# Performance work log

Hardware: AMD Instinct MI355X
Metric: run time of the kernel (lower is better)

The kernel has to match this reference:

```python
import jax, jax.numpy as jnp
import numpy as np
import math

HID = 2048; NH = 16; NKV = 4; NG = NH // NKV
LORA = 512; D_ROPE = 64; D_NOPE = 128; D_V = 128
D_QK = D_NOPE + D_ROPE  # 192
B, S = 2, 2048
ROPE_BASE = 10000.0


def setup_inputs() -> dict:
    key = jax.random.key(0)
    ks = jax.random.split(key, 5)
    s = lambda fan_in: 1.0 / math.sqrt(fan_in)
    return {
        "hidden_states": jax.random.normal(ks[0], (B, S, HID), jnp.float32),
        "Wqkv": jax.random.uniform(ks[1], (HID, NH * D_QK + LORA), jnp.float32, -s(HID), s(HID)),
        "Wk_up": jax.random.uniform(ks[2], (LORA, NKV * D_QK), jnp.float32, -s(LORA), s(LORA)),
        "Wv_up": jax.random.uniform(ks[3], (LORA, NKV * D_V), jnp.float32, -s(LORA), s(LORA)),
        "Wo": jax.random.uniform(ks[4], (NH * D_V, HID), jnp.float32, -s(NH * D_V), s(NH * D_V)),
    }


def _rope(x, seq_len):
    # x: [b, s, h, D_ROPE]; standard rotate-half RoPE
    inv_freq = 1.0 / (ROPE_BASE ** (jnp.arange(0, D_ROPE, 2, dtype=jnp.float32) / D_ROPE))
    t = jnp.arange(seq_len, dtype=jnp.float32)
    freqs = jnp.outer(t, inv_freq)                      # [s, D_ROPE/2]
    emb = jnp.concatenate([freqs, freqs], axis=-1)      # [s, D_ROPE]
    cos = jnp.cos(emb)[None, :, None, :].astype(x.dtype)
    sin = jnp.sin(emb)[None, :, None, :].astype(x.dtype)
    x1, x2 = jnp.split(x, 2, axis=-1)
    rot = jnp.concatenate([-x2, x1], axis=-1)
    return x * cos + rot * sin


def reference(hidden_states, Wqkv, Wk_up, Wv_up, Wo):
    b, s, _ = hidden_states.shape
    qkv = hidden_states @ Wqkv                              # [b,s,NH*D_QK+LORA]
    q, c_kv = jnp.split(qkv, [NH * D_QK], axis=-1)
    q = q.reshape(b, s, NH, D_QK)
    k = (c_kv @ Wk_up).reshape(b, s, NKV, D_QK)
    v = (c_kv @ Wv_up).reshape(b, s, NKV, D_V)
    q_nope, q_rope = jnp.split(q, [D_NOPE], axis=-1)
    k_nope, k_rope = jnp.split(k, [D_NOPE], axis=-1)
    q = jnp.concatenate([q_nope, _rope(q_rope, s)], axis=-1)   # [b,s,NH,D_QK]
    k = jnp.concatenate([k_nope, _rope(k_rope, s)], axis=-1)   # [b,s,NKV,D_QK]
    # GQA broadcast: repeat_interleave kv heads to NH
    k = jnp.repeat(k, NG, axis=2)
    v = jnp.repeat(v, NG, axis=2)
    scale = 1.0 / math.sqrt(D_QK)
    scores = jnp.einsum("bqhd,bkhd->bhqk", q, k) * scale
    causal = jnp.tril(jnp.ones((s, s), bool))
    scores = jnp.where(causal[None, None], scores, jnp.finfo(scores.dtype).min)
    probs = jax.nn.softmax(scores, axis=-1)
    out = jnp.einsum("bhqk,bkhd->bqhd", probs, v).reshape(b, s, NH * D_V)
    return out @ Wo
```

## Files before the change

kernel.cpp:

```cpp
#include <hip/hip_runtime.h>
#include <hip/hip_bf16.h>
#include <math.h>

#define HIDN  2048
#define NH    16
#define NKV   4
#define LORA  512
#define D_ROPE 64
#define D_NOPE 128
#define D_VV  128
#define D_QKD 192
#define BATCH 2
#define SEQ   2048
#define NTOK  (BATCH*SEQ)
#define QKV_W (NH*D_QKD + LORA)
#define KW    (NKV*D_QKD)
#define VW    (NKV*D_VV)
#define AW    (NH*D_VV)
#define QSCALE 0.07216878364870323f
#define LOG2E  1.4426950408889634f

typedef __attribute__((ext_vector_type(8))) __bf16 bf16x8;
typedef __attribute__((ext_vector_type(4))) float f32x4;

static __device__ __forceinline__ unsigned short f2bf(float f) {
    unsigned int u = __builtin_bit_cast(unsigned int, f);
    u += 0x7fffu + ((u >> 16) & 1u);
    return (unsigned short)(u >> 16);
}
static __device__ __forceinline__ float bf2f(unsigned short v) {
    unsigned int u = (unsigned int)v << 16;
    return __builtin_bit_cast(float, u);
}
static __device__ __forceinline__ unsigned int cvt_pk_bf16(float lo, float hi) {
    unsigned int r;
    asm("v_cvt_pk_bf16_f32 %0, %1, %2" : "=v"(r) : "v"(lo), "v"(hi));
    return r;
}
static __device__ __forceinline__ void gl2lds16(const unsigned short* g, unsigned short* l) {
    __builtin_amdgcn_global_load_lds(
        (const __attribute__((address_space(1))) unsigned int*)g,
        (__attribute__((address_space(3))) unsigned int*)l, 16, 0, 0);
}

__global__ __launch_bounds__(256) void transpose_w(
    const float* __restrict__ W, unsigned short* __restrict__ Wt,
    int K, int N, int scale_ncols, float scale)
{
    __shared__ float T[64][68];
    const int tid = threadIdx.x;
    const int k0 = blockIdx.y * 64, n0 = blockIdx.x * 64;
    const int rr = tid >> 4;
    const int c4 = (tid & 15) * 4;

#pragma unroll
    for (int i = 0; i < 4; ++i) {
        int r = rr + 16 * i;
        *(float4*)&T[r][c4] = *(const float4*)&W[(size_t)(k0 + r) * N + n0 + c4];
    }
    __syncthreads();
#pragma unroll
    for (int i = 0; i < 4; ++i) {
        int nr = rr + 16 * i;
        float sc = (n0 + nr < scale_ncols) ? scale : 1.0f;
        unsigned short tmp[4];
#pragma unroll
        for (int j = 0; j < 4; ++j) tmp[j] = f2bf(T[c4 + j][nr] * sc);
        unsigned int p0 = (unsigned int)tmp[0] | ((unsigned int)tmp[1] << 16);
        unsigned int p1 = (unsigned int)tmp[2] | ((unsigned int)tmp[3] << 16);
        *(uint2*)&Wt[(size_t)(n0 + nr) * K + k0 + c4] = make_uint2(p0, p1);
    }
}

__global__ __launch_bounds__(256) void cast_plain(const float* __restrict__ src,
                                                  unsigned short* __restrict__ dst)
{
    int idx = blockIdx.x * 256 + threadIdx.x;
    float4 v = *(const float4*)&src[(size_t)idx * 4];
    unsigned int p0 = (unsigned int)f2bf(v.x) | ((unsigned int)f2bf(v.y) << 16);
    unsigned int p1 = (unsigned int)f2bf(v.z) | ((unsigned int)f2bf(v.w) << 16);
    *(uint2*)&dst[(size_t)idx * 4] = make_uint2(p0, p1);
}

template<int OUT_MODE>
__global__ __launch_bounds__(256) void gemm_bt(
    const unsigned short* __restrict__ A,
    const unsigned short* __restrict__ Bt,
    void* __restrict__ C,
    int K, int lda, int ldb, int ldc)
{
    __shared__ __align__(16) unsigned short As[128 * 32];
    __shared__ __align__(16) unsigned short Bs[128 * 32];

    const int tid  = threadIdx.x;
    const int w    = tid >> 6;
    const int lane = tid & 63;
    const int quad = lane >> 4;
    const int l15  = lane & 15;
    const int brow = blockIdx.y * 128;
    const int bcol = blockIdx.x * 128;
    const int wr   = (w >> 1) * 64;
    const int wc   = (w & 1) * 64;

    const int srow = lane >> 2;
    const int sseg = (lane & 3) * 8;
    const int r0   = w * 32;

    f32x4 acc[4][4];
#pragma unroll
    for (int mt = 0; mt < 4; ++mt)
#pragma unroll
        for (int nt = 0; nt < 4; ++nt) acc[mt][nt] = (f32x4){0.f, 0.f, 0.f, 0.f};

    const unsigned short* Ab = A  + (size_t)(brow + r0 + srow) * lda + sseg;
    const unsigned short* Bb = Bt + (size_t)(bcol + r0 + srow) * ldb + sseg;

    for (int k0 = 0; k0 < K; k0 += 32) {
        __syncthreads();
        gl2lds16(Ab + k0,                     As + r0 * 32);
        gl2lds16(Ab + k0 + (size_t)16 * lda,  As + (r0 + 16) * 32);
        gl2lds16(Bb + k0,                     Bs + r0 * 32);
        gl2lds16(Bb + k0 + (size_t)16 * ldb,  Bs + (r0 + 16) * 32);
        __syncthreads();

        bf16x8 af[4], bfr[4];
#pragma unroll
        for (int mt = 0; mt < 4; ++mt)
            af[mt] = __builtin_bit_cast(bf16x8,
                *(const uint4*)(As + (wr + mt * 16 + l15) * 32 + quad * 8));
#pragma unroll
        for (int nt = 0; nt < 4; ++nt)
            bfr[nt] = __builtin_bit_cast(bf16x8,
                *(const uint4*)(Bs + (wc + nt * 16 + l15) * 32 + quad * 8));
#pragma unroll
        for (int mt = 0; mt < 4; ++mt)
#pragma unroll
            for (int nt = 0; nt < 4; ++nt)
                acc[mt][nt] = __builtin_amdgcn_mfma_f32_16x16x32_bf16(
                    af[mt], bfr[nt], acc[mt][nt], 0, 0, 0);
    }

    if (OUT_MODE == 2) {
#pragma unroll
        for (int mt = 0; mt < 4; ++mt) {
            int row0 = brow + wr + mt * 16 + quad * 4;
            int r5   = row0 & 31;
            int pos  = ((r5 & 15) >> 2) * 8 + ((r5 >> 4) << 2);
            int prow0 = (row0 & ~31) | pos;
#pragma unroll
            for (int nt = 0; nt < 4; ++nt) {
                int col = bcol + wc + nt * 16 + l15;
                unsigned int p0 = (unsigned int)f2bf(acc[mt][nt][0]) |
                                  ((unsigned int)f2bf(acc[mt][nt][1]) << 16);
                unsigned int p1 = (unsigned int)f2bf(acc[mt][nt][2]) |
                                  ((unsigned int)f2bf(acc[mt][nt][3]) << 16);
                *(uint2*)&((unsigned short*)C)[(size_t)col * ldc + prow0] = make_uint2(p0, p1);
            }
        }
    } else {
#pragma unroll
        for (int mt = 0; mt < 4; ++mt)
#pragma unroll
            for (int i = 0; i < 4; ++i) {
                size_t row = (size_t)(brow + wr + mt * 16 + quad * 4 + i);
#pragma unroll
                for (int nt = 0; nt < 4; ++nt) {
                    int col = bcol + wc + nt * 16 + l15;
                    ((unsigned short*)C)[row * ldc + col] = f2bf(acc[mt][nt][i]);
                }
            }
    }
}

template<int OUT_MODE, int BN>
__global__ __launch_bounds__(512, 2) void gemm8p(
    const unsigned short* __restrict__ A,
    const unsigned short* __restrict__ Bt,
    void* __restrict__ C,
    int K, int lda, int ldb, int ldc)
{
    constexpr int BNF = BN / 64;
    constexpr int LB  = BN / 64;
    constexpr int HB  = LB / 2;
    constexpr int ASLOT = 256 * 64;
    constexpr int BSLOT = BN * 64;
    constexpr int SLOT  = ASLOT + BSLOT;
    constexpr int NW  = 3 + 2 * HB;

    extern __shared__ __align__(16) unsigned short lds[];

    const int tid  = threadIdx.x;
    const int w    = tid >> 6;
    const int lane = tid & 63;
    const int quad = lane >> 4;
    const int l15  = lane & 15;
    const int wm   = w >> 2;
    const int wn   = w & 3;

    int fid = blockIdx.y * gridDim.x + blockIdx.x;
    int nwg = gridDim.x * gridDim.y;
    int cpx = nwg >> 3;
    int swz = (fid & 7) * cpx + (fid >> 3);
    int bx  = swz % gridDim.x;
    int by  = swz / gridDim.x;
    const int brow = by * 256;
    const int bcol = bx * BN;

    const unsigned short* Ab = A  + (size_t)brow * lda;
    const unsigned short* Bb = Bt + (size_t)bcol * ldb;

    const int lr   = lane >> 3;
    const int lswz = ((lane & 7) ^ lr) * 8;
    const int arow0 = (w < 4) ? (w * 8) : (128 + (w - 4) * 8);
    const int asrc  = (arow0 + lr) * lda + lswz;
    int brow0[HB], bsrc[HB];
#pragma unroll
    for (int c = 0; c < HB; ++c) {
        brow0[c] = (w * HB + c) * 8;
        bsrc[c]  = (brow0[c] + lr) * ldb + lswz;
    }

    f32x4 acc[8][BNF];
#pragma unroll
    for (int mf = 0; mf < 8; ++mf)
#pragma unroll
        for (int nf = 0; nf < BNF; ++nf) acc[mf][nf] = (f32x4){0.f, 0.f, 0.f, 0.f};

    const int NT = K >> 6;

    auto stageA = [&](int s, int tt, int p) {
        gl2lds16(Ab + tt * 64 + p * 32 * lda + asrc,
                 lds + s * SLOT + (arow0 + p * 32) * 64);
    };
    auto stageB = [&](int s, int tt, int h) {
#pragma unroll
        for (int c = 0; c < HB; ++c)
            gl2lds16(Bb + tt * 64 + h * (BN / 2) * ldb + bsrc[c],
                     lds + s * SLOT + ASLOT + (brow0[c] + h * (BN / 2)) * 64);
    };

    stageB(0, 0, 0); stageB(0, 0, 1);
    stageA(0, 0, 0); stageA(0, 0, 1); stageA(0, 0, 2);
    stageB(1, 1, 0);
    stageA(0, 0, 3);
    stageB(1, 1, 1);
    asm volatile("s_waitcnt vmcnt(%0)" :: "i"(NW) : "memory");
    __builtin_amdgcn_s_barrier();

#pragma unroll 1
    for (int t = 0; t < NT; ++t) {
        const int s  = t & 1;
        const int s1 = s ^ 1;
        const int t1 = (t + 1 < NT) ? t + 1 : 0;
        const int t2 = (t + 2 < NT) ? t + 2 : t + 2 - NT;
        const unsigned short* As = lds + s * SLOT;
        const unsigned short* Bs = As + ASLOT;

        bf16x8 bq[BNF][2], af[2][2];

#pragma unroll
        for (int ph = 0; ph < 4; ++ph) {
            if (ph == 0) {
#pragma unroll
                for (int nf = 0; nf < BNF; ++nf)
#pragma unroll
                    for (int kk = 0; kk < 2; ++kk) {
                        int r = wn * (BN / 4) + nf * 16 + l15;
                        bq[nf][kk] = __builtin_bit_cast(bf16x8,
                            *(const uint4*)(Bs + r * 64 + (((kk * 4 + quad) ^ (r & 7)) * 8)));
                    }
            }
#pragma unroll
            for (int m = 0; m < 2; ++m)
#pragma unroll
                for (int kk = 0; kk < 2; ++kk) {
                    int r = wm * 128 + (ph * 2 + m) * 16 + l15;
                    af[m][kk] = __builtin_bit_cast(bf16x8,
                        *(const uint4*)(As + r * 64 + (((kk * 4 + quad) ^ (r & 7)) * 8)));
                }
            stageA(s1, t1, ph);
            if (ph == 2) stageB(s, t2, 0);
            if (ph == 3) stageB(s, t2, 1);
            __builtin_amdgcn_s_barrier();
            __builtin_amdgcn_s_setprio(1);
#pragma unroll
            for (int m = 0; m < 2; ++m)
#pragma unroll
                for (int nf = 0; nf < BNF; ++nf)
#pragma unroll
                    for (int kk = 0; kk < 2; ++kk)
                        acc[ph * 2 + m][nf] = __builtin_amdgcn_mfma_f32_16x16x32_bf16(
                            af[m][kk], bq[nf][kk], acc[ph * 2 + m][nf], 0, 0, 0);
            __builtin_amdgcn_s_setprio(0);
            asm volatile("s_waitcnt vmcnt(%0)" :: "i"(NW) : "memory");
            __builtin_amdgcn_s_barrier();
        }
    }
    asm volatile("s_waitcnt vmcnt(0)" ::: "memory");

#pragma unroll
    for (int mf = 0; mf < 8; ++mf) {
#pragma unroll
        for (int i = 0; i < 4; ++i) {
            size_t row = (size_t)(brow + wm * 128 + mf * 16 + quad * 4 + i);
#pragma unroll
            for (int nf = 0; nf < BNF; ++nf) {
                int col = bcol + wn * (BN / 4) + nf * 16 + l15;
                if (OUT_MODE == 1)
                    ((unsigned short*)C)[row * ldc + col] = f2bf(acc[mf][nf][i]);
                else
                    ((float*)C)[row * ldc + col] = acc[mf][nf][i];
            }
        }
    }
}

__global__ __launch_bounds__(256) void rope_bf16(unsigned short* __restrict__ qkvb,
                                                 unsigned short* __restrict__ kb)
{
    int idx = blockIdx.x * 256 + threadIdx.x;
    int i    = idx & 31;
    int head = (idx >> 5) % 20;
    int t    = idx / (20 * 32);
    if (t >= NTOK) return;
    int pos = t & (SEQ - 1);

    const float LOG_BASE_OVER_32 = 0.28782313662425572f;
    float ang = (float)pos * __expf(-(float)i * LOG_BASE_OVER_32);
    float c = cosf(ang);
    float sn = sinf(ang);

    unsigned short* p;
    if (head < NH) p = qkvb + (size_t)t * QKV_W + head * D_QKD + D_NOPE;
    else           p = kb   + (size_t)t * KW    + (head - NH) * D_QKD + D_NOPE;

    float x1 = bf2f(p[i]), x2 = bf2f(p[i + 32]);
    p[i]      = f2bf(x1 * c - x2 * sn);
    p[i + 32] = f2bf(x2 * c + x1 * sn);
}

__global__ __launch_bounds__(256) void attn_mfma(
    const unsigned short* __restrict__ qkvb,
    const unsigned short* __restrict__ kb,
    const unsigned short* __restrict__ vt,
    unsigned short* __restrict__ attnb)
{
    __shared__ __align__(16) unsigned short KsL[2 * 32 * 192];
    __shared__ __align__(16) unsigned short VtL[2 * 128 * 32];

    const int tid  = threadIdx.x;
    const int w    = tid >> 6;
    const int lane = tid & 63;
    const int quad = lane >> 4;
    const int l15  = lane & 15;

    const int bid = blockIdx.x;
    const int g   = bid >> 5;
    const int jj  = g & 7;
    const int m   = g >> 3;
    int qt;
    if      (m == 0) qt = 31 - jj;
    else if (m == 1) qt = 16 + jj;
    else if (m == 2) qt = 15 - jj;
    else             qt = jj;
    const int hb = bid & 31;
    const int h  = hb & 15;
    const int b  = hb >> 4;
    const int kvh = h >> 2;

    const int x7   = l15 & 7;
    const int vx   = (l15 >> 1) & 3;

    int koff[3], voff[2];
#pragma unroll
    for (int it = 0; it < 3; ++it) {
        int bidx = (w * 3 + it) * 64 + lane;
        int row  = bidx / 24;
        int sblk = bidx - row * 24;
        int gblk = sblk ^ (row & 7);
        koff[it] = row * KW + gblk * 8;
    }
#pragma unroll
    for (int it = 0; it < 2; ++it) {
        int bidx = (w * 2 + it) * 64 + lane;
        int row  = bidx >> 2;
        int gblk = (bidx & 3) ^ ((row >> 1) & 3);
        voff[it] = row * NTOK + gblk * 8;
    }
    const unsigned short* kp0 = kb + (size_t)(b * SEQ) * KW + kvh * D_QKD;
    const unsigned short* vp0 = vt + (size_t)(kvh * 128) * NTOK + b * SEQ;

    const int q0   = qt * 64;
    const int q0w  = q0 + w * 16;
    const int wmax = q0w + 15;

    bf16x8 qf[6];
    {
        const unsigned short* qp =
            qkvb + (size_t)(b * SEQ + q0w + l15) * QKV_W + h * D_QKD + quad * 8;
#pragma unroll
        for (int t = 0; t < 6; ++t)
            qf[t] = __builtin_bit_cast(bf16x8, *(const uint4*)(qp + t * 32));
    }

    f32x4 o[8];
#pragma unroll
    for (int c = 0; c < 8; ++c) o[c] = (f32x4){0.f, 0.f, 0.f, 0.f};
    float lp = 0.f;

    const int nt = 2 * qt + 2;

    {
#pragma unroll
        for (int it = 0; it < 3; ++it)
            gl2lds16(kp0 + koff[it], KsL + (w * 3 + it) * 512);
#pragma unroll
        for (int it = 0; it < 2; ++it)
            gl2lds16(vp0 + voff[it], VtL + (w * 2 + it) * 512);
    }
    __syncthreads();

    for (int tk = 0; tk < nt; ++tk) {
        const int k0  = tk * 32;
        const int cur = tk & 1;

        if (tk + 1 < nt) {
            const int nxt = cur ^ 1;
            const unsigned short* ks = kp0 + (size_t)(k0 + 32) * KW;
            const unsigned short* vs = vp0 + (k0 + 32);
#pragma unroll
            for (int it = 0; it < 3; ++it)
                gl2lds16(ks + koff[it], KsL + nxt * (32 * 192) + (w * 3 + it) * 512);
#pragma unroll
            for (int it = 0; it < 2; ++it)
                gl2lds16(vs + voff[it], VtL + nxt * (128 * 32) + (w * 2 + it) * 512);
        }

        if (k0 <= wmax) {
            const unsigned short* Kc = KsL + cur * (32 * 192);
            const unsigned short* Vc = VtL + cur * (128 * 32);

            f32x4 s[2];
            __builtin_amdgcn_s_setprio(1);
#pragma unroll
            for (int j = 0; j < 2; ++j) {
                f32x4 acc = {0.f, 0.f, 0.f, 0.f};
                const unsigned short* kr = Kc + (j * 16 + l15) * 192;
#pragma unroll
                for (int t = 0; t < 6; ++t) {
                    int sblk = (quad + 4 * t) ^ x7;
                    bf16x8 kf = __builtin_bit_cast(bf16x8, *(const uint4*)(kr + sblk * 8));
                    acc = __builtin_amdgcn_mfma_f32_16x16x32_bf16(kf, qf[t], acc, 0, 0, 0);
                }
                s[j] = acc;
            }
            __builtin_amdgcn_s_setprio(0);

            if (k0 + 31 <= q0w) {
#pragma unroll
                for (int j = 0; j < 2; ++j)
#pragma unroll
                    for (int i = 0; i < 4; ++i) {
                        float p = __builtin_amdgcn_exp2f(s[j][i]);
                        s[j][i] = p;
                        lp += p;
                    }
            } else {
                const int qrow = q0w + l15;
#pragma unroll
                for (int j = 0; j < 2; ++j)
#pragma unroll
                    for (int i = 0; i < 4; ++i) {
                        int kidx = k0 + j * 16 + quad * 4 + i;
                        float p = (kidx <= qrow) ? __builtin_amdgcn_exp2f(s[j][i]) : 0.f;
                        s[j][i] = p;
                        lp += p;
                    }
            }

            uint4 pk;
            pk.x = cvt_pk_bf16(s[0][0], s[0][1]);
            pk.y = cvt_pk_bf16(s[0][2], s[0][3]);
            pk.z = cvt_pk_bf16(s[1][0], s[1][1]);
            pk.w = cvt_pk_bf16(s[1][2], s[1][3]);
            bf16x8 pa = __builtin_bit_cast(bf16x8, pk);

            __builtin_amdgcn_s_setprio(1);
#pragma unroll
            for (int c = 0; c < 8; ++c) {
                bf16x8 vf = __builtin_bit_cast(bf16x8,
                    *(const uint4*)(Vc + (c * 16 + l15) * 32 + ((quad ^ vx) * 8)));
                o[c] = __builtin_amdgcn_mfma_f32_16x16x32_bf16(pa, vf, o[c], 0, 0, 0);
            }
            __builtin_amdgcn_s_setprio(0);
        }

        __syncthreads();
    }

    float lt = lp;
    lt += __shfl_xor(lt, 16);
    lt += __shfl_xor(lt, 32);

#pragma unroll
    for (int i = 0; i < 4; ++i) {
        float inv = 1.0f / __shfl(lt, (lane & 48) | (quad * 4 + i));
        size_t rowoff = (size_t)(b * SEQ + q0w + quad * 4 + i) * AW + h * D_VV + l15;
#pragma unroll
        for (int c = 0; c < 8; ++c)
            attnb[rowoff + c * 16] = f2bf(o[c][i] * inv);
    }
}

extern "C" void kernel_launch(void* const* d_in, const int* in_sizes, int n_in,
                              void* d_out, int out_size, void* d_ws, size_t ws_size,
                              hipStream_t stream)
{
    const float* X     = (const float*)d_in[0];
    const float* Wqkv  = (const float*)d_in[1];
    const float* Wk_up = (const float*)d_in[2];
    const float* Wv_up = (const float*)d_in[3];
    const float* Wo    = (const float*)d_in[4];
    float* out = (float*)d_out;

    unsigned short* Xb    = (unsigned short*)d_ws;
    unsigned short* Wqt   = Xb    + (size_t)NTOK * HIDN;
    unsigned short* Wkt   = Wqt   + (size_t)QKV_W * HIDN;
    unsigned short* Wvt   = Wkt   + (size_t)KW * LORA;
    unsigned short* Wot   = Wvt   + (size_t)VW * LORA;
    unsigned short* qkvb  = Wot   + (size_t)HIDN * AW;
    unsigned short* kb    = qkvb  + (size_t)NTOK * QKV_W;
    unsigned short* vtb   = kb    + (size_t)NTOK * KW;
    unsigned short* attnb = vtb   + (size_t)VW * NTOK;

    cast_plain<<<NTOK * HIDN / 4 / 256, 256, 0, stream>>>(X, Xb);
    transpose_w<<<dim3(QKV_W / 64, HIDN / 64), 256, 0, stream>>>(
        Wqkv, Wqt, HIDN, QKV_W, NH * D_QKD, QSCALE * LOG2E);
    transpose_w<<<dim3(KW / 64, LORA / 64), 256, 0, stream>>>(Wk_up, Wkt, LORA, KW, 0, 1.0f);
    transpose_w<<<dim3(VW / 64, LORA / 64), 256, 0, stream>>>(Wv_up, Wvt, LORA, VW, 0, 1.0f);
    transpose_w<<<dim3(AW / 64, HIDN / 64), 256, 0, stream>>>(Wo, Wot, HIDN, AW, 0, 1.0f);

    gemm8p<1, 256><<<dim3(QKV_W / 256, NTOK / 256), 512, 131072, stream>>>(
        Xb, Wqt, qkvb, HIDN, HIDN, HIDN, QKV_W);

    gemm_bt<1><<<dim3(KW / 128, NTOK / 128), 256, 0, stream>>>(
        qkvb + NH * D_QKD, Wkt, kb, LORA, QKV_W, LORA, KW);
    gemm_bt<2><<<dim3(VW / 128, NTOK / 128), 256, 0, stream>>>(
        qkvb + NH * D_QKD, Wvt, vtb, LORA, QKV_W, LORA, NTOK);

    rope_bf16<<<(NTOK * 20 * 32 + 255) / 256, 256, 0, stream>>>(qkvb, kb);

    attn_mfma<<<dim3(1024), 256, 0, stream>>>(qkvb, kb, vtb, attnb);

    gemm8p<0, 128><<<dim3(HIDN / 128, NTOK / 256), 512, 98304, stream>>>(
        attnb, Wot, out, AW, AW, AW, HIDN);
}
```

Before: 334.9 us.

## Enlarge attention query tile to 128 rows with XCD-aware block mapping

The attention kernel now runs 512 blocks of 512 threads. Each block covers 128 query rows with 8 waves instead of 64 rows with 4 waves, so every K/V tile loaded into LDS is reused by twice as many queries. Block IDs are remapped so that blocks with the same (batch, kv-head) land on the same XCD, which should improve L2 reuse of K/V. Six waves now load K and two waves load V. The trade-off is fewer, larger blocks, which can worsen load balance across the causal triangle and raise per-CU register and occupancy pressure.

```diff
diff --git a/kernel.cpp b/kernel.cpp
--- a/kernel.cpp
+++ b/kernel.cpp
@@ -339,7 +339,7 @@
     p[i + 32] = f2bf(x2 * c + x1 * sn);
 }
 
-__global__ __launch_bounds__(256) void attn_mfma(
+__global__ __launch_bounds__(512) void attn_mfma(
     const unsigned short* __restrict__ qkvb,
     const unsigned short* __restrict__ kb,
     const unsigned short* __restrict__ vt,
@@ -355,34 +355,30 @@
     const int l15  = lane & 15;
 
     const int bid = blockIdx.x;
-    const int g   = bid >> 5;
-    const int jj  = g & 7;
-    const int m   = g >> 3;
-    int qt;
-    if      (m == 0) qt = 31 - jj;
-    else if (m == 1) qt = 16 + jj;
-    else if (m == 2) qt = 15 - jj;
-    else             qt = jj;
-    const int hb = bid & 31;
-    const int h  = hb & 15;
-    const int b  = hb >> 4;
-    const int kvh = h >> 2;
+    const int xcd = bid & 7;
+    const int kvh = xcd >> 1;
+    const int b   = xcd & 1;
+    const int rest = bid >> 3;
+    const int h   = kvh * 4 + (rest & 3);
+    const int g   = rest >> 2;
+    const int qt  = (g < 8) ? (15 - g) : (g - 8);
+    const int q0  = qt * 128;
 
     const int x7   = l15 & 7;
     const int vx   = (l15 >> 1) & 3;
 
-    int koff[3], voff[2];
-#pragma unroll
-    for (int it = 0; it < 3; ++it) {
-        int bidx = (w * 3 + it) * 64 + lane;
+    int koff[2], voff[4];
+#pragma unroll
+    for (int it = 0; it < 2; ++it) {
+        int bidx = ((w - 2) * 2 + it) * 64 + lane;
         int row  = bidx / 24;
         int sblk = bidx - row * 24;
         int gblk = sblk ^ (row & 7);
         koff[it] = row * KW + gblk * 8;
     }
 #pragma unroll
-    for (int it = 0; it < 2; ++it) {
-        int bidx = (w * 2 + it) * 64 + lane;
+    for (int it = 0; it < 4; ++it) {
+        int bidx = (w * 4 + it) * 64 + lane;
         int row  = bidx >> 2;
         int gblk = (bidx & 3) ^ ((row >> 1) & 3);
         voff[it] = row * NTOK + gblk * 8;
@@ -390,7 +386,6 @@
     const unsigned short* kp0 = kb + (size_t)(b * SEQ) * KW + kvh * D_QKD;
     const unsigned short* vp0 = vt + (size_t)(kvh * 128) * NTOK + b * SEQ;
 
-    const int q0   = qt * 64;
     const int q0w  = q0 + w * 16;
     const int wmax = q0w + 15;
 
@@ -408,15 +403,16 @@
     for (int c = 0; c < 8; ++c) o[c] = (f32x4){0.f, 0.f, 0.f, 0.f};
     float lp = 0.f;
 
-    const int nt = 2 * qt + 2;
-
-    {
-#pragma unroll
-        for (int it = 0; it < 3; ++it)
-            gl2lds16(kp0 + koff[it], KsL + (w * 3 + it) * 512);
+    const int nt = 4 * qt + 4;
+
+    if (w >= 2) {
 #pragma unroll
         for (int it = 0; it < 2; ++it)
-            gl2lds16(vp0 + voff[it], VtL + (w * 2 + it) * 512);
+            gl2lds16(kp0 + koff[it], KsL + ((w - 2) * 2 + it) * 512);
+    } else {
+#pragma unroll
+        for (int it = 0; it < 4; ++it)
+            gl2lds16(vp0 + voff[it], VtL + (w * 4 + it) * 512);
     }
     __syncthreads();
 
@@ -426,14 +422,17 @@
 
         if (tk + 1 < nt) {
             const int nxt = cur ^ 1;
-            const unsigned short* ks = kp0 + (size_t)(k0 + 32) * KW;
-            const unsigned short* vs = vp0 + (k0 + 32);
-#pragma unroll
-            for (int it = 0; it < 3; ++it)
-                gl2lds16(ks + koff[it], KsL + nxt * (32 * 192) + (w * 3 + it) * 512);
-#pragma unroll
-            for (int it = 0; it < 2; ++it)
-                gl2lds16(vs + voff[it], VtL + nxt * (128 * 32) + (w * 2 + it) * 512);
+            if (w >= 2) {
+                const unsigned short* ks = kp0 + (size_t)(k0 + 32) * KW;
+#pragma unroll
+                for (int it = 0; it < 2; ++it)
+                    gl2lds16(ks + koff[it], KsL + nxt * (32 * 192) + ((w - 2) * 2 + it) * 512);
+            } else {
+                const unsigned short* vs = vp0 + (k0 + 32);
+#pragma unroll
+                for (int it = 0; it < 4; ++it)
+                    gl2lds16(vs + voff[it], VtL + nxt * (128 * 32) + (w * 4 + it) * 512);
+            }
         }
 
         if (k0 <= wmax) {
@@ -550,7 +549,7 @@
 
     rope_bf16<<<(NTOK * 20 * 32 + 255) / 256, 256, 0, stream>>>(qkvb, kb);
 
-    attn_mfma<<<dim3(1024), 256, 0, stream>>>(qkvb, kb, vtb, attnb);
+    attn_mfma<<<dim3(512), 512, 0, stream>>>(qkvb, kb, vtb, attnb);
 
     gemm8p<0, 128><<<dim3(HIDN / 128, NTOK / 256), 512, 98304, stream>>>(
         attnb, Wot, out, AW, AW, AW, HIDN);
```

Result: faster. 326.2 us (-2.6%).
